# Optimization experiments

Measured on AMD Instinct MI355X. Metric: run time of the kernel, lower is better.

The kernel has to match this reference:

```python
import jax, jax.numpy as jnp
import numpy as np

SEQ, EMB, QKV = 4096, 1024, 1024

def setup_inputs() -> dict:
    key = jax.random.key(0)
    k_x, k_q, k_k, k_v = jax.random.split(key, 4)
    scale = 1.0 / np.sqrt(EMB)
    return {
        "x": jax.random.normal(k_x, (SEQ, EMB), dtype=jnp.float32),
        "W_q": jax.random.normal(k_q, (EMB, QKV), dtype=jnp.float32) * scale,
        "W_k": jax.random.normal(k_k, (EMB, QKV), dtype=jnp.float32) * scale,
        "W_v": jax.random.normal(k_v, (EMB, QKV), dtype=jnp.float32) * scale,
    }

def reference(x, W_q, W_k, W_v):
    # Single-head scaled dot-product attention, unbatched: x [S, E]
    d_k = W_q.shape[1]
    Q = x @ W_q          # [S, D]
    K = x @ W_k          # [S, D]
    V = x @ W_v          # [S, D]
    scores = (Q @ K.T) * (1.0 / jnp.sqrt(jnp.asarray(d_k, dtype=x.dtype)))  # [S, S]
    attn = jax.nn.softmax(scores, axis=-1)
    return attn @ V      # [S, D]
```

## Files before the change

### kernel.cpp

```cpp
#include <hip/hip_runtime.h>
#include <cstdint>

#define S_DIM 4096
#define E_DIM 1024
#define D_DIM 1024

typedef __bf16 bf16x8 __attribute__((ext_vector_type(8)));
typedef float  f32x4  __attribute__((ext_vector_type(4)));
typedef unsigned short u16x8 __attribute__((ext_vector_type(8)));

__device__ __forceinline__ unsigned short f2bf(float f) {
  unsigned u = __float_as_uint(f);
  unsigned r = (u + 0x7fffu + ((u >> 16) & 1u)) >> 16;
  return (unsigned short)r;
}

__device__ __forceinline__ void lds_copy16(const unsigned short* g, const unsigned short* l) {
  auto gp = reinterpret_cast<__attribute__((address_space(1))) unsigned int*>(
      reinterpret_cast<uintptr_t>(g));
  auto lp = reinterpret_cast<__attribute__((address_space(3))) unsigned int*>(
      reinterpret_cast<uintptr_t>(l));
  __builtin_amdgcn_global_load_lds(gp, lp, 16, 0, 0);
}

__global__ __launch_bounds__(256) void prep_kernel(
    const float* __restrict__ x,
    const float* __restrict__ Wq, const float* __restrict__ Wk, const float* __restrict__ Wv,
    unsigned short* __restrict__ xbf, unsigned short* __restrict__ Wt,
    float* __restrict__ lsum) {
  const int z = blockIdx.z;
  const int tid = threadIdx.x;
  if (z < 3) {
    const float* W = (z == 0) ? Wq : (z == 1 ? Wk : Wv);
    unsigned short* out = Wt + (size_t)z * E_DIM * D_DIM;
    __shared__ unsigned short tile[32][33];
    int bc = blockIdx.x * 32, br = blockIdx.y * 32;
    int tx = tid & 31, ty = tid >> 5;
#pragma unroll
    for (int i = 0; i < 32; i += 8)
      tile[ty + i][tx] = f2bf(W[(size_t)(br + ty + i) * D_DIM + bc + tx]);
    __syncthreads();
#pragma unroll
    for (int i = 0; i < 32; i += 8)
      out[(size_t)(bc + ty + i) * E_DIM + br + tx] = tile[tx][ty + i];
  } else {
    int bid = blockIdx.y * 32 + blockIdx.x;
    int i = (bid * 256 + tid) * 16;
#pragma unroll
    for (int h = 0; h < 2; h++) {
      float4 a = *(const float4*)(x + i + h * 8);
      float4 b = *(const float4*)(x + i + h * 8 + 4);
      u16x8 o;
      o[0] = f2bf(a.x); o[1] = f2bf(a.y); o[2] = f2bf(a.z); o[3] = f2bf(a.w);
      o[4] = f2bf(b.x); o[5] = f2bf(b.y); o[6] = f2bf(b.z); o[7] = f2bf(b.w);
      *(u16x8*)(xbf + i + h * 8) = o;
    }
    if (bid < 16) lsum[bid * 256 + tid] = 0.f;
  }
}

template <int MODE, int NSPLIT, int BN, int BK>
__device__ __forceinline__ void gemm_body(
    const unsigned short* __restrict__ A, int lda,
    const unsigned short* __restrict__ Bt, int ldb,
    void* __restrict__ Cp, unsigned short* __restrict__ C1, int ldc,
    int Kper, float scale, float* __restrict__ lsum,
    int bm, int bn, unsigned short* sA, unsigned short* sB) {
  constexpr int NF = BN / 32;
  constexpr int NC = BK / 8;
  constexpr int RP = 2048 / BK;
  constexpr int PA = 128 / RP;
  constexpr int PB = BN / RP;
  constexpr int HH = BK / 32;

  const int tid = threadIdx.x;
  const int wave = tid >> 6;
  const int lane = tid & 63;
  const int q    = lane >> 4;
  const int l16  = lane & 15;
  const int lx   = l16 & 7;
  const int wm   = (wave >> 1) * 64;
  const int wn   = (wave & 1) * (BN / 2);

  f32x4 zero = {0.f, 0.f, 0.f, 0.f};
  f32x4 acc[4][NF];
#pragma unroll
  for (int t = 0; t < 4; t++)
#pragma unroll
    for (int u = 0; u < NF; u++) acc[t][u] = zero;

  const int srow   = tid / NC;
  const int schunk = (tid % NC) ^ (srow & 7);
  const unsigned short* ap = A  + (size_t)(bm + srow) * lda + schunk * 8;
  const unsigned short* bp = Bt + (size_t)(bn + srow) * ldb + schunk * 8;
  unsigned short* saw = sA + wave * 512;
  unsigned short* sbw = sB + wave * 512;
  const size_t stepA = (size_t)RP * lda;
  const size_t stepB = (size_t)RP * ldb;

  for (int k0 = 0; k0 < Kper; k0 += BK) {
#pragma unroll
    for (int p = 0; p < PA; p++)
      lds_copy16(ap + k0 + p * stepA, saw + p * 2048);
#pragma unroll
    for (int p = 0; p < PB; p++)
      lds_copy16(bp + k0 + p * stepB, sbw + p * 2048);
    __syncthreads();

#pragma unroll
    for (int h = 0; h < HH; h++) {
      bf16x8 af[4], bfv[NF];
      const int pc = (((h << 2) | q) ^ lx) * 8;
#pragma unroll
      for (int t = 0; t < 4; t++)
        af[t] = *reinterpret_cast<const bf16x8*>(sA + (wm + t * 16 + l16) * BK + pc);
#pragma unroll
      for (int u = 0; u < NF; u++)
        bfv[u] = *reinterpret_cast<const bf16x8*>(sB + (wn + u * 16 + l16) * BK + pc);
#pragma unroll
      for (int t = 0; t < 4; t++)
#pragma unroll
        for (int u = 0; u < NF; u++)
          acc[t][u] = __builtin_amdgcn_mfma_f32_16x16x32_bf16(af[t], bfv[u], acc[t][u], 0, 0, 0);
    }
    __syncthreads();
  }

  unsigned short* cb16 = (unsigned short*)Cp;
  int coloff = bn;
  if constexpr (NSPLIT == 2) {
    if (bn >= 1024) cb16 = C1;
    coloff = bn & 1023;
  }
  float* o32 = (float*)Cp;

#pragma unroll
  for (int t = 0; t < 4; t++) {
#pragma unroll
    for (int rr = 0; rr < 4; rr++) {
      const int row = bm + wm + t * 16 + q * 4 + rr;
      float invl = 1.0f;
      if constexpr (MODE == 2) invl = 1.0f / lsum[row];
      float rs = 0.f;
#pragma unroll
      for (int u = 0; u < NF; u++) {
        const int col = coloff + wn + u * 16 + l16;
        float v = acc[t][u][rr] * scale;
        if constexpr (MODE == 0) {
          cb16[(size_t)row * ldc + col] = f2bf(v);
        } else if constexpr (MODE == 1) {
          float p = __expf(v - 8.0f);
          rs += p;
          cb16[(size_t)row * ldc + col] = f2bf(p);
        } else {
          o32[(size_t)row * ldc + col] = acc[t][u][rr] * invl;
        }
      }
      if constexpr (MODE == 1) {
        rs += __shfl_xor(rs, 1);
        rs += __shfl_xor(rs, 2);
        rs += __shfl_xor(rs, 4);
        rs += __shfl_xor(rs, 8);
        if (l16 == 0) unsafeAtomicAdd(&lsum[row], rs);
      }
    }
  }
}

__global__ __launch_bounds__(256, 2) void proj_gemm(
    const unsigned short* __restrict__ xbf, const unsigned short* __restrict__ Wt,
    unsigned short* __restrict__ Qbf, unsigned short* __restrict__ Kbf,
    unsigned short* __restrict__ Vt) {
  __shared__ __align__(16) unsigned short sA[128 * 64];
  __shared__ __align__(16) unsigned short sB[128 * 64];
  const int idx = blockIdx.x;
  if (idx < 512) {
    int g = idx >> 7, r = idx & 127;
    int bm = (g * 8 + (r & 7)) * 128, bn = (r >> 3) * 128;
    gemm_body<0, 2, 128, 64>(xbf, E_DIM, Wt, E_DIM, Qbf, Kbf, D_DIM,
                             E_DIM, 1.0f, nullptr, bm, bn, sA, sB);
  } else {
    int r = idx - 512;
    int bm = (r & 7) * 128, bn = (r >> 3) * 128;
    gemm_body<0, 1, 128, 64>(Wt + 2 * E_DIM * D_DIM, E_DIM, xbf, E_DIM, Vt,
                             nullptr, S_DIM, E_DIM, 1.0f, nullptr, bm, bn, sA, sB);
  }
}

__global__ __launch_bounds__(256, 2) void s_gemm(
    const unsigned short* __restrict__ Q, const unsigned short* __restrict__ K,
    unsigned short* __restrict__ SP, float* __restrict__ lsum) {
  __shared__ __align__(16) unsigned short sA[128 * 64];
  __shared__ __align__(16) unsigned short sB[128 * 64];
  int flat = blockIdx.y * gridDim.x + blockIdx.x;
  int numInG = 8 * gridDim.x;
  int g = flat / numInG;
  int r = flat - g * numInG;
  int bm = (g * 8 + (r & 7)) * 128, bn = (r >> 3) * 128;
  gemm_body<1, 1, 128, 64>(Q, D_DIM, K, D_DIM, SP, nullptr, S_DIM,
                           D_DIM, 0.03125f, lsum, bm, bn, sA, sB);
}

__global__ __launch_bounds__(256, 2) void o_gemm(
    const unsigned short* __restrict__ SP, const unsigned short* __restrict__ Vt,
    float* __restrict__ out, const float* __restrict__ lsum) {
  __shared__ __align__(16) unsigned short sA[128 * 128];
  __shared__ __align__(16) unsigned short sB[64 * 128];
  int flat = blockIdx.y * gridDim.x + blockIdx.x;
  int numInG = 8 * gridDim.x;
  int g = flat / numInG;
  int r = flat - g * numInG;
  int bm = (g * 8 + (r & 7)) * 128, bn = (r >> 3) * 64;
  gemm_body<2, 1, 64, 128>(SP, S_DIM, Vt, S_DIM, out, nullptr, D_DIM,
                           S_DIM, 1.0f, (float*)lsum, bm, bn, sA, sB);
}

extern "C" void kernel_launch(void* const* d_in, const int* in_sizes, int n_in,
                              void* d_out, int out_size, void* d_ws, size_t ws_size,
                              hipStream_t stream) {
  const float* x  = (const float*)d_in[0];
  const float* Wq = (const float*)d_in[1];
  const float* Wk = (const float*)d_in[2];
  const float* Wv = (const float*)d_in[3];
  float* out = (float*)d_out;

  char* ws = (char*)d_ws;
  const size_t MB = 1024 * 1024;
  unsigned short* SP   = (unsigned short*)(ws);
  unsigned short* xbf  = (unsigned short*)(ws + 8 * MB);
  unsigned short* Wt   = (unsigned short*)(ws + 16 * MB);
  unsigned short* Qbf  = (unsigned short*)(ws + 32 * MB);
  unsigned short* Kbf  = (unsigned short*)(ws + 40 * MB);
  unsigned short* Vt   = (unsigned short*)(ws + 48 * MB);
  float*          lsum = (float*)(ws + 56 * MB);

  dim3 blk(256);

  dim3 prgrid(32, 32, 4);
  prep_kernel<<<prgrid, blk, 0, stream>>>(x, Wq, Wk, Wv, xbf, Wt, lsum);

  proj_gemm<<<dim3(768), blk, 0, stream>>>(xbf, Wt, Qbf, Kbf, Vt);

  dim3 sgrid(32, 32);
  s_gemm<<<sgrid, blk, 0, stream>>>(Qbf, Kbf, SP, lsum);

  dim3 ogrid(16, 32);
  o_gemm<<<ogrid, blk, 0, stream>>>(SP, Vt, out, lsum);
}
```

Measured before the change: 206.0 us.

## Move V projection into the score GEMM launch to balance kernel stages

```diff
diff --git a/kernel.cpp b/kernel.cpp
--- a/kernel.cpp
+++ b/kernel.cpp
@@ -167,38 +167,37 @@
   }
 }
 
-__global__ __launch_bounds__(256, 2) void proj_gemm(
+__global__ __launch_bounds__(256, 2) void qk_gemm(
     const unsigned short* __restrict__ xbf, const unsigned short* __restrict__ Wt,
-    unsigned short* __restrict__ Qbf, unsigned short* __restrict__ Kbf,
-    unsigned short* __restrict__ Vt) {
+    unsigned short* __restrict__ Qbf, unsigned short* __restrict__ Kbf) {
   __shared__ __align__(16) unsigned short sA[128 * 64];
   __shared__ __align__(16) unsigned short sB[128 * 64];
-  const int idx = blockIdx.x;
-  if (idx < 512) {
-    int g = idx >> 7, r = idx & 127;
-    int bm = (g * 8 + (r & 7)) * 128, bn = (r >> 3) * 128;
-    gemm_body<0, 2, 128, 64>(xbf, E_DIM, Wt, E_DIM, Qbf, Kbf, D_DIM,
-                             E_DIM, 1.0f, nullptr, bm, bn, sA, sB);
-  } else {
-    int r = idx - 512;
-    int bm = (r & 7) * 128, bn = (r >> 3) * 128;
-    gemm_body<0, 1, 128, 64>(Wt + 2 * E_DIM * D_DIM, E_DIM, xbf, E_DIM, Vt,
-                             nullptr, S_DIM, E_DIM, 1.0f, nullptr, bm, bn, sA, sB);
-  }
-}
-
-__global__ __launch_bounds__(256, 2) void s_gemm(
-    const unsigned short* __restrict__ Q, const unsigned short* __restrict__ K,
-    unsigned short* __restrict__ SP, float* __restrict__ lsum) {
+  const int bid = blockIdx.x;
+  const int g = bid >> 7, r = bid & 127;
+  gemm_body<0, 2, 128, 64>(xbf, E_DIM, Wt, E_DIM, Qbf, Kbf, D_DIM,
+                           E_DIM, 1.0f, nullptr,
+                           (g * 8 + (r & 7)) * 128, (r >> 3) * 128, sA, sB);
+}
+
+__global__ __launch_bounds__(256, 2) void sv_gemm(
+    const unsigned short* __restrict__ xbf, const unsigned short* __restrict__ Wt,
+    const unsigned short* __restrict__ Qbf, const unsigned short* __restrict__ Kbf,
+    unsigned short* __restrict__ Vt, unsigned short* __restrict__ SP,
+    float* __restrict__ lsum) {
   __shared__ __align__(16) unsigned short sA[128 * 64];
   __shared__ __align__(16) unsigned short sB[128 * 64];
-  int flat = blockIdx.y * gridDim.x + blockIdx.x;
-  int numInG = 8 * gridDim.x;
-  int g = flat / numInG;
-  int r = flat - g * numInG;
-  int bm = (g * 8 + (r & 7)) * 128, bn = (r >> 3) * 128;
-  gemm_body<1, 1, 128, 64>(Q, D_DIM, K, D_DIM, SP, nullptr, S_DIM,
-                           D_DIM, 0.03125f, lsum, bm, bn, sA, sB);
+  const int bid = blockIdx.x;
+  if (bid < 256) {
+    gemm_body<0, 1, 128, 64>(Wt + 2 * E_DIM * D_DIM, E_DIM, xbf, E_DIM, Vt,
+                             nullptr, S_DIM, E_DIM, 1.0f, nullptr,
+                             (bid & 7) * 128, (bid >> 3) * 128, sA, sB);
+  } else {
+    const int idx = bid - 256;
+    const int g = idx >> 8, r = idx & 255;
+    gemm_body<1, 1, 128, 64>(Qbf, D_DIM, Kbf, D_DIM, SP, nullptr, S_DIM,
+                             D_DIM, 0.03125f, lsum,
+                             (g * 8 + (r & 7)) * 128, (r >> 3) * 128, sA, sB);
+  }
 }
 
 __global__ __launch_bounds__(256, 2) void o_gemm(
@@ -239,10 +238,9 @@
   dim3 prgrid(32, 32, 4);
   prep_kernel<<<prgrid, blk, 0, stream>>>(x, Wq, Wk, Wv, xbf, Wt, lsum);
 
-  proj_gemm<<<dim3(768), blk, 0, stream>>>(xbf, Wt, Qbf, Kbf, Vt);
-
-  dim3 sgrid(32, 32);
-  s_gemm<<<sgrid, blk, 0, stream>>>(Qbf, Kbf, SP, lsum);
+  qk_gemm<<<dim3(512), blk, 0, stream>>>(xbf, Wt, Qbf, Kbf);
+
+  sv_gemm<<<dim3(1280), blk, 0, stream>>>(xbf, Wt, Qbf, Kbf, Vt, SP, lsum);
 
   dim3 ogrid(16, 32);
   o_gemm<<<ogrid, blk, 0, stream>>>(SP, Vt, out, lsum);
```

New measurement: 204.1 us. About the same (-0.9%).
